# Optimization experiments

Measured on AMD Instinct MI355X. Metric: run time of the kernel, lower is better.

Reference implementation:

```python
import jax, jax.numpy as jnp
import numpy as np

B, S, H = 64, 2048, 1024
INPUT_SCALE = 100.0
DT = 0.01


def setup_inputs() -> dict:
    key = jax.random.key(0)
    ks = jax.random.split(key, 16)
    def vec(k, scale=0.5):
        return jax.random.normal(k, (H,), jnp.float32) * scale
    x_codes = 65.0 + 10.0 * jax.random.normal(ks[0], (B, S), jnp.float32)
    return {
        "x_codes": x_codes,
        "Wi_w": vec(ks[1]), "Wi_b": vec(ks[2], 0.1),
        "Wf_w": vec(ks[3]), "Wf_b": vec(ks[4], 0.1),
        "Wo_w": vec(ks[5]), "Wo_b": vec(ks[6], 0.1),
        "Wg_w": vec(ks[7]), "Wg_b": vec(ks[8], 0.1),
        "Wl_w": vec(ks[9]), "Wl_b": vec(ks[10], 0.1),
        "proj_w": jax.random.normal(ks[11], (2, H), jnp.float32) * 0.03,
        "proj_b": jnp.zeros((2,), jnp.float32),
        "n_init": jnp.zeros((H,), jnp.float32),
    }


def reference(x_codes, Wi_w, Wi_b, Wf_w, Wf_b, Wo_w, Wo_b, Wg_w, Wg_b,
              Wl_w, Wl_b, proj_w, proj_b, n_init):
    b, s = x_codes.shape
    h0 = jnp.zeros((b, H), x_codes.dtype)
    c0 = jnp.zeros_like(h0)
    n0 = jnp.broadcast_to(n_init, (b, H))
    x = (x_codes - 65.0) / INPUT_SCALE          # [B,S]
    xs = x.T[:, :, None]                         # [S,B,1] scan over time

    def step(carry, xt):
        h, c, n = carry
        pre_i = xt * Wi_w + Wi_b                 # [B,H] (Linear(1,H))
        pre_f = xt * Wf_w + Wf_b
        pre_o = xt * Wo_w + Wo_b
        pre_g = xt * Wg_w + Wg_b
        lam = jax.nn.sigmoid(xt * Wl_w + Wl_b)
        i_t = jnp.exp(pre_i - n)
        f_t = jnp.exp(pre_f - n)
        o_t = jnp.exp(pre_o - n)
        g_t = jax.nn.sigmoid(pre_g)              # act_g == 'sigmoid'
        c_new = f_t * c + i_t * g_t
        ff = o_t * jax.nn.sigmoid(c_new)         # act_c == 'sigmoid'
        h_new = (h + DT * ff) / (1.0 + DT * lam)
        n_new = n + 0.01 * (i_t + f_t + o_t - 3.0)
        y = h_new @ proj_w.T + proj_b            # [B,2]
        return (h_new, c_new, n_new), y

    _, ys = jax.lax.scan(step, (h0, c0, n0), xs)  # ys: [S,B,2]
    return ys.transpose(1, 0, 2)                  # [B,S,2]
```

## Files before the change

### kernel.cpp

```cpp
#include <hip/hip_runtime.h>


#define Bv   64
#define Sv   2048
#define Hv   1024
#define TPB  256
#define NT   512
#define CH   16
#define HSTR 17
#define HBUF (TPB * HSTR)

#define L2E   1.44269504088896340736f
#define NL2E (-1.44269504088896340736f)
#define LN2   0.69314718055994530942f
#define KNU   0.014426950408889634f
#define CREB  0.692493619626702435f
#define LOG2_001 (-6.6438561897747247f)

__device__ __forceinline__ float fexp2(float x) { return __builtin_amdgcn_exp2f(x); }
__device__ __forceinline__ float frcp(float x)  { return __builtin_amdgcn_rcpf(x); }

__global__ __launch_bounds__(256) void init_out(const float* __restrict__ proj_b,
                                                float* __restrict__ out) {
    int i = blockIdx.x * 256 + threadIdx.x;
    out[i] = proj_b[i & 1];
}

__global__ __launch_bounds__(NT, 1) void cfc_scan(
    const float* __restrict__ x_codes,
    const float* __restrict__ Wi_w, const float* __restrict__ Wi_b,
    const float* __restrict__ Wf_w, const float* __restrict__ Wf_b,
    const float* __restrict__ Wo_w, const float* __restrict__ Wo_b,
    const float* __restrict__ Wg_w, const float* __restrict__ Wg_b,
    const float* __restrict__ Wl_w, const float* __restrict__ Wl_b,
    const float* __restrict__ proj_w,
    const float* __restrict__ n_init,
    float* __restrict__ out)
{
    __shared__ float hlds[2 * HBUF];
    __shared__ float pwlds[2 * TPB];

    const int b   = blockIdx.x >> 2;
    const int q   = blockIdx.x & 3;
    const int tid = threadIdx.x;

    const float* __restrict__ xrow = x_codes + b * Sv;
    float* __restrict__ orow = out + b * (Sv * 2);

    const int ct   = tid - TPB;
    const int rk   = (ct >> 7) & 1;
    const int rt   = (ct >> 3) & 15;
    const int rseg = ct & 7;
    if (tid >= TPB) {
        pwlds[ct]       = proj_w[q * TPB + ct];
        pwlds[TPB + ct] = proj_w[Hv + q * TPB + ct];
    }

    float wi2 = 0, bi2 = 0, wf2 = 0, bf2 = 0, wo2 = 0, bo2 = 0;
    float wg2 = 0, bg2 = 0, wl2 = 0, bl2 = 0;
    float m = 0, En = 0, C = 0, h = 0;
    if (tid < TPB) {
        const int j = q * TPB + tid;
        const float wi = Wi_w[j], bi = Wi_b[j];
        const float wf = Wf_w[j], bf = Wf_b[j];
        const float wo = Wo_w[j], bo = Wo_b[j];
        const float wg = Wg_w[j], bg = Wg_b[j];
        const float wl = Wl_w[j], bl = Wl_b[j];
        wi2 = wi * KNU;  bi2 = fmaf(-0.65f, wi, bi) * L2E;
        wf2 = wf * KNU;  bf2 = fmaf(-0.65f, wf, bf) * L2E;
        wo2 = wo * KNU;  bo2 = fmaf(-0.65f, wo, bo) * L2E + LOG2_001;
        wg2 = -wg * KNU; bg2 = fmaf(-0.65f, wg, bg) * NL2E;
        wl2 = -wl * KNU; bl2 = fmaf(-0.65f, wl, bl) * NL2E;
        m  = n_init[j] * NL2E;
        En = fexp2(m);
    }

    float Gf[CH], GiGg[CH], Goa[CH], Gs[CH], Il[CH];

    static const float CUP[CH] = {
        1.0f,        1.03045453f, 1.06183655f, 1.09417428f,
        1.12749685f, 1.16183424f, 1.19721736f, 1.23367806f,
        1.27124915f, 1.30996445f, 1.34985881f, 1.39096813f,
        1.43332941f, 1.47698079f, 1.52196156f, 1.56831219f };

    int par = 0;
    for (int t0 = 0; t0 < Sv; t0 += CH, par ^= 1) {
        if (tid < TPB) {
            #pragma unroll
            for (int u = 0; u < CH; ++u) {
                const float xc = xrow[t0 + u];
                const float Gi = fexp2(fmaf(xc, wi2, bi2));
                Gf[u]  = fexp2(fmaf(xc, wf2, bf2));
                Goa[u] = fexp2(fmaf(xc, wo2, bo2));
                const float eg = fexp2(fmaf(xc, wg2, bg2));
                const float Gg = frcp(fmaf(eg, -LN2, -LN2));
                GiGg[u] = Gi * Gg;
                const float el = fexp2(fmaf(xc, wl2, bl2));
                Il[u]   = fmaf(frcp(el + 1.01f), -0.01f, 1.0f);
                Gs[u]   = fmaf(Goa[u], 100.0f, Gi + Gf[u]);
            }
            float* __restrict__ hrow = &hlds[par * HBUF + tid * HSTR];
            #pragma unroll
            for (int u = 0; u < CH; ++u) {
                const float Enu = (u == 0) ? En : En * CUP[u];
                const float ef  = Gf[u] * Enu;
                C = fmaf(ef, C, GiGg[u] * Enu);
                const float sc = frcp(1.0f + fexp2(C));
                h = fmaf(Goa[u] * Enu, sc, h) * Il[u];
                hrow[u] = h;
                m = fmaf(Gs[u] * Enu, -KNU, m);
                if (u == CH - 1) m += CREB;
                En = fexp2(m);
            }
        }
        __syncthreads();
        if (tid >= TPB) {
            const float* __restrict__ hb  = &hlds[par * HBUF];
            const float* __restrict__ pwk = &pwlds[rk * TPB];
            float sum = 0.0f;
            #pragma unroll
            for (int i2 = 0; i2 < 32; ++i2) {
                const int v  = (i2 + 4 * rseg) & 31;
                const int jj = rseg * 32 + v;
                sum = fmaf(hb[jj * HSTR + rt], pwk[jj], sum);
            }
            sum += __shfl_xor(sum, 1, 64);
            sum += __shfl_xor(sum, 2, 64);
            sum += __shfl_xor(sum, 4, 64);
            if (rseg == 0) atomicAdd(&orow[(t0 + rt) * 2 + rk], sum);
        }
    }
}

extern "C" void kernel_launch(void* const* d_in, const int* in_sizes, int n_in,
                              void* d_out, int out_size, void* d_ws, size_t ws_size,
                              hipStream_t stream) {
    const float* x_codes = (const float*)d_in[0];
    const float* Wi_w = (const float*)d_in[1];
    const float* Wi_b = (const float*)d_in[2];
    const float* Wf_w = (const float*)d_in[3];
    const float* Wf_b = (const float*)d_in[4];
    const float* Wo_w = (const float*)d_in[5];
    const float* Wo_b = (const float*)d_in[6];
    const float* Wg_w = (const float*)d_in[7];
    const float* Wg_b = (const float*)d_in[8];
    const float* Wl_w = (const float*)d_in[9];
    const float* Wl_b = (const float*)d_in[10];
    const float* proj_w = (const float*)d_in[11];
    const float* proj_b = (const float*)d_in[12];
    const float* n_init = (const float*)d_in[13];
    float* out = (float*)d_out;

    init_out<<<out_size / 256, 256, 0, stream>>>(proj_b, out);
    cfc_scan<<<Bv * (Hv / TPB), NT, 0, stream>>>(
        x_codes, Wi_w, Wi_b, Wf_w, Wf_b, Wo_w, Wo_b, Wg_w, Wg_b, Wl_w, Wl_b,
        proj_w, n_init, out);
}
```

Baseline: 261.2 us.

## Split recurrence into three-stage pipeline across producer and consumer warps

Reworks the scan into a three-stage software pipeline. The first 256 threads compute the gate exponentials and the normalizer recurrence, then write pre-scaled f, i*g and o terms to double-buffered LDS. The second 256 threads run the C/h recurrence with the lambda gate one chunk behind, and project h two chunks behind with proj_w held in registers. This spreads the transcendental work across both halves of the block instead of leaving consumer warps idle, at the cost of more LDS traffic, a larger LDS footprint and two extra pipeline iterations.

```diff
diff --git a/kernel.cpp b/kernel.cpp
--- a/kernel.cpp
+++ b/kernel.cpp
@@ -7,8 +7,9 @@
 #define TPB  256
 #define NT   512
 #define CH   16
-#define HSTR 17
-#define HBUF (TPB * HSTR)
+#define NCH  (Sv / CH)
+#define STR  17
+#define ROWS (TPB * STR)
 
 #define L2E   1.44269504088896340736f
 #define NL2E (-1.44269504088896340736f)
@@ -37,45 +38,53 @@
     const float* __restrict__ n_init,
     float* __restrict__ out)
 {
-    __shared__ float hlds[2 * HBUF];
-    __shared__ float pwlds[2 * TPB];
+    __shared__ float Pb[2][ROWS];
+    __shared__ float Fb[2][ROWS];
+    __shared__ float Ob[2][ROWS];
+    __shared__ float Hb[2][ROWS];
 
     const int b   = blockIdx.x >> 2;
     const int q   = blockIdx.x & 3;
     const int tid = threadIdx.x;
+    const int ct  = tid - TPB;
 
     const float* __restrict__ xrow = x_codes + b * Sv;
     float* __restrict__ orow = out + b * (Sv * 2);
 
-    const int ct   = tid - TPB;
-    const int rk   = (ct >> 7) & 1;
-    const int rt   = (ct >> 3) & 15;
-    const int rseg = ct & 7;
-    if (tid >= TPB) {
-        pwlds[ct]       = proj_w[q * TPB + ct];
-        pwlds[TPB + ct] = proj_w[Hv + q * TPB + ct];
-    }
+    float wi2 = 0, bi2 = 0, wf2 = 0, bf2 = 0, wo2 = 0, bo2 = 0;
+    float wg2 = 0, bg2 = 0;
+    float m = 0, En = 0;
+    float wl2 = 0, bl2 = 0;
+    float C = 0, h = 0;
+    float pwreg[32];
+    int   rk = 0, rt = 0, rseg = 0;
 
-    float wi2 = 0, bi2 = 0, wf2 = 0, bf2 = 0, wo2 = 0, bo2 = 0;
-    float wg2 = 0, bg2 = 0, wl2 = 0, bl2 = 0;
-    float m = 0, En = 0, C = 0, h = 0;
     if (tid < TPB) {
         const int j = q * TPB + tid;
         const float wi = Wi_w[j], bi = Wi_b[j];
         const float wf = Wf_w[j], bf = Wf_b[j];
         const float wo = Wo_w[j], bo = Wo_b[j];
         const float wg = Wg_w[j], bg = Wg_b[j];
-        const float wl = Wl_w[j], bl = Wl_b[j];
         wi2 = wi * KNU;  bi2 = fmaf(-0.65f, wi, bi) * L2E;
         wf2 = wf * KNU;  bf2 = fmaf(-0.65f, wf, bf) * L2E;
         wo2 = wo * KNU;  bo2 = fmaf(-0.65f, wo, bo) * L2E + LOG2_001;
         wg2 = -wg * KNU; bg2 = fmaf(-0.65f, wg, bg) * NL2E;
-        wl2 = -wl * KNU; bl2 = fmaf(-0.65f, wl, bl) * NL2E;
         m  = n_init[j] * NL2E;
         En = fexp2(m);
+    } else {
+        const int j = q * TPB + ct;
+        const float wl = Wl_w[j], bl = Wl_b[j];
+        wl2 = -wl * KNU; bl2 = fmaf(-0.65f, wl, bl) * NL2E;
+        rk   = (ct >> 7) & 1;
+        rt   = (ct >> 3) & 15;
+        rseg = ct & 7;
+        const float* __restrict__ pwsrc = proj_w + rk * Hv + q * TPB;
+        #pragma unroll
+        for (int i2 = 0; i2 < 32; ++i2) {
+            const int jj = rseg * 32 + ((i2 + 4 * rseg) & 31);
+            pwreg[i2] = pwsrc[jj];
+        }
     }
-
-    float Gf[CH], GiGg[CH], Goa[CH], Gs[CH], Il[CH];
 
     static const float CUP[CH] = {
         1.0f,        1.03045453f, 1.06183655f, 1.09417428f,
@@ -83,52 +92,66 @@
         1.27124915f, 1.30996445f, 1.34985881f, 1.39096813f,
         1.43332941f, 1.47698079f, 1.52196156f, 1.56831219f };
 
-    int par = 0;
-    for (int t0 = 0; t0 < Sv; t0 += CH, par ^= 1) {
+    for (int c = 0; c < NCH + 2; ++c) {
         if (tid < TPB) {
-            #pragma unroll
-            for (int u = 0; u < CH; ++u) {
-                const float xc = xrow[t0 + u];
-                const float Gi = fexp2(fmaf(xc, wi2, bi2));
-                Gf[u]  = fexp2(fmaf(xc, wf2, bf2));
-                Goa[u] = fexp2(fmaf(xc, wo2, bo2));
-                const float eg = fexp2(fmaf(xc, wg2, bg2));
-                const float Gg = frcp(fmaf(eg, -LN2, -LN2));
-                GiGg[u] = Gi * Gg;
-                const float el = fexp2(fmaf(xc, wl2, bl2));
-                Il[u]   = fmaf(frcp(el + 1.01f), -0.01f, 1.0f);
-                Gs[u]   = fmaf(Goa[u], 100.0f, Gi + Gf[u]);
+            if (c < NCH) {
+                const int t0 = c * CH;
+                float* __restrict__ Pp = &Pb[c & 1][tid * STR];
+                float* __restrict__ Fp = &Fb[c & 1][tid * STR];
+                float* __restrict__ Op = &Ob[c & 1][tid * STR];
+                #pragma unroll
+                for (int u = 0; u < CH; ++u) {
+                    const float xc  = xrow[t0 + u];
+                    const float Gi  = fexp2(fmaf(xc, wi2, bi2));
+                    const float Gf  = fexp2(fmaf(xc, wf2, bf2));
+                    const float Goa = fexp2(fmaf(xc, wo2, bo2));
+                    const float eg  = fexp2(fmaf(xc, wg2, bg2));
+                    const float Gg  = frcp(fmaf(eg, -LN2, -LN2));
+                    const float Enu = (u == 0) ? En : En * CUP[u];
+                    Fp[u] = Gf * Enu;
+                    Pp[u] = (Gi * Gg) * Enu;
+                    Op[u] = Goa * Enu;
+                    const float Gs = fmaf(Goa, 100.0f, Gi + Gf);
+                    m = fmaf(Gs * Enu, -KNU, m);
+                    if (u == CH - 1) m += CREB;
+                    En = fexp2(m);
+                }
             }
-            float* __restrict__ hrow = &hlds[par * HBUF + tid * HSTR];
-            #pragma unroll
-            for (int u = 0; u < CH; ++u) {
-                const float Enu = (u == 0) ? En : En * CUP[u];
-                const float ef  = Gf[u] * Enu;
-                C = fmaf(ef, C, GiGg[u] * Enu);
-                const float sc = frcp(1.0f + fexp2(C));
-                h = fmaf(Goa[u] * Enu, sc, h) * Il[u];
-                hrow[u] = h;
-                m = fmaf(Gs[u] * Enu, -KNU, m);
-                if (u == CH - 1) m += CREB;
-                En = fexp2(m);
+        } else {
+            if (c >= 1 && c <= NCH) {
+                const int d  = c - 1;
+                const int t0 = d * CH;
+                const float* __restrict__ Pp = &Pb[d & 1][ct * STR];
+                const float* __restrict__ Fp = &Fb[d & 1][ct * STR];
+                const float* __restrict__ Op = &Ob[d & 1][ct * STR];
+                float* __restrict__ Hp = &Hb[d & 1][ct * STR];
+                #pragma unroll
+                for (int u = 0; u < CH; ++u) {
+                    const float xc = xrow[t0 + u];
+                    const float el = fexp2(fmaf(xc, wl2, bl2));
+                    const float Il = fmaf(frcp(el + 1.01f), -0.01f, 1.0f);
+                    C = fmaf(Fp[u], C, Pp[u]);
+                    const float sc = frcp(1.0f + fexp2(C));
+                    h = fmaf(Op[u], sc, h) * Il;
+                    Hp[u] = h;
+                }
+            }
+            if (c >= 2) {
+                const int e  = c - 2;
+                const float* __restrict__ hb = &Hb[e & 1][0];
+                float sum = 0.0f;
+                #pragma unroll
+                for (int i2 = 0; i2 < 32; ++i2) {
+                    const int jj = rseg * 32 + ((i2 + 4 * rseg) & 31);
+                    sum = fmaf(hb[jj * STR + rt], pwreg[i2], sum);
+                }
+                sum += __shfl_xor(sum, 1, 64);
+                sum += __shfl_xor(sum, 2, 64);
+                sum += __shfl_xor(sum, 4, 64);
+                if (rseg == 0) atomicAdd(&orow[(e * CH + rt) * 2 + rk], sum);
             }
         }
         __syncthreads();
-        if (tid >= TPB) {
-            const float* __restrict__ hb  = &hlds[par * HBUF];
-            const float* __restrict__ pwk = &pwlds[rk * TPB];
-            float sum = 0.0f;
-            #pragma unroll
-            for (int i2 = 0; i2 < 32; ++i2) {
-                const int v  = (i2 + 4 * rseg) & 31;
-                const int jj = rseg * 32 + v;
-                sum = fmaf(hb[jj * HSTR + rt], pwk[jj], sum);
-            }
-            sum += __shfl_xor(sum, 1, 64);
-            sum += __shfl_xor(sum, 2, 64);
-            sum += __shfl_xor(sum, 4, 64);
-            if (rseg == 0) atomicAdd(&orow[(t0 + rt) * 2 + rk], sum);
-        }
     }
 }
 
```

After: 320.6 us. 22.7% more time.
